# Kernel tuning notes

Measured on AMD Instinct MI355X. Metric: run time of the kernel, lower is better.

Reference implementation:

```python
import jax, jax.numpy as jnp
import numpy as np

N = 100000        # nodes
E = 1600000       # edges
D = 32            # hidden dim
C = 2             # num classes
NL = 4            # layer_num - 1 GIN layers
G = 512           # graphs in batch
BN_EPS = 1e-3     # keras BatchNormalization default epsilon


def setup_inputs() -> dict:
    key = jax.random.key(0)
    ks = jax.random.split(key, 16)
    s = 0.1
    return {
        "node_embeddings": jax.random.normal(ks[0], (N, D), dtype=jnp.float32),
        "edge_index": jax.random.randint(ks[1], (2, E), 0, N, dtype=jnp.int32),
        "batch": jnp.sort(jax.random.randint(ks[2], (N,), 0, G, dtype=jnp.int32)),
        # MLP inner dense + BN (per GIN layer)
        "W1": jax.random.normal(ks[3], (NL, D, D), dtype=jnp.float32) * s,
        "b1": jnp.zeros((NL, D), jnp.float32),
        "bn1_g": jnp.ones((NL, D), jnp.float32),
        "bn1_b": jnp.zeros((NL, D), jnp.float32),
        # MLP output dense
        "W2": jax.random.normal(ks[4], (NL, D, D), dtype=jnp.float32) * s,
        "b2": jnp.zeros((NL, D), jnp.float32),
        # ApplyNodeFunc BN
        "bn2_g": jnp.ones((NL, D), jnp.float32),
        "bn2_b": jnp.zeros((NL, D), jnp.float32),
        # outer per-layer BN
        "norm_g": jnp.ones((NL, D), jnp.float32),
        "norm_b": jnp.zeros((NL, D), jnp.float32),
        # readout heads: one Dense(num_classes) per hidden_rep level (layer_num of them)
        "dense_W": jax.random.normal(ks[5], (NL + 1, D, C), dtype=jnp.float32) * s,
        "dense_b": jnp.zeros((NL + 1, C), jnp.float32),
    }


def _bn(x, g, b):
    # inference-mode BatchNorm with init moving stats (mean=0, var=1)
    return x * (g / jnp.sqrt(1.0 + BN_EPS)) + b


def reference(node_embeddings, edge_index, batch, W1, b1, bn1_g, bn1_b,
              W2, b2, bn2_g, bn2_b, norm_g, norm_b, dense_W, dense_b):
    src, dst = edge_index[0], edge_index[1]
    h = node_embeddings
    hidden = [h]
    for i in range(NL):
        # GIN aggregation: (1+eps)*h + sum of neighbor features (eps=0)
        agg = jax.ops.segment_sum(h[src], dst, num_segments=N)  # [N, D]
        z = h + agg
        # ApplyNodeFunc: MLP (Dense->BN->ReLU->Dense) then BN + ReLU
        z = jax.nn.relu(_bn(z @ W1[i] + b1[i], bn1_g[i], bn1_b[i]))
        z = z @ W2[i] + b2[i]
        z = jax.nn.relu(_bn(z, bn2_g[i], bn2_b[i]))
        # outer norm + relu
        h = jax.nn.relu(_bn(z, norm_g[i], norm_b[i]))
        hidden.append(h)
    # readout: segment-sum pooling per hidden level, Dense(num_classes), summed
    score = jnp.zeros((G, C), dtype=node_embeddings.dtype)
    for i, hr in enumerate(hidden):
        pool = jax.ops.segment_sum(hr, batch, num_segments=G)  # [G, D]
        score = score + pool @ dense_W[i] + dense_b[i]
    return jax.nn.softmax(score, axis=-1)
```

## Files before the change

### kernel.cpp

```cpp
#include <hip/hip_runtime.h>

#define NN 100000
#define EE 1600000
#define DD 32
#define CC 2
#define NLAYERS 4
#define GG 512

#define BW 1024
#define NBUK ((NN + BW - 1) / BW)
#define CAP 24576
#define CH 8192
#define NPART ((EE + CH - 1) / CH)

__global__ void part_kernel(const int* __restrict__ ei,
                            int* __restrict__ gcur,
                            unsigned* __restrict__ part) {
    __shared__ unsigned sorted[CH];
    __shared__ unsigned char sbkt[CH];
    __shared__ int cnt[NBUK], offs[NBUK], cur[NBUK], gbs[NBUK];

    const int tid = threadIdx.x;
    const int eb  = blockIdx.x * CH;
    const int nch = min(CH, EE - eb);

    for (int b = tid; b < NBUK; b += 256) cnt[b] = 0;
    __syncthreads();
    for (int i = tid; i < nch; i += 256) {
        int dn = ei[EE + eb + i];
        atomicAdd(&cnt[dn >> 10], 1);
    }
    __syncthreads();
    if (tid == 0) {
        int o = 0;
        for (int b = 0; b < NBUK; ++b) { offs[b] = o; o += cnt[b]; }
    }
    __syncthreads();
    if (tid < NBUK) {
        cur[tid] = offs[tid];
        gbs[tid] = cnt[tid] ? atomicAdd(&gcur[tid], cnt[tid]) : 0;
    }
    __syncthreads();
    for (int i = tid; i < nch; i += 256) {
        int s  = ei[eb + i];
        int dn = ei[EE + eb + i];
        int b  = dn >> 10;
        unsigned pk = ((unsigned)(dn & (BW - 1)) << 17) | (unsigned)s;
        int p = atomicAdd(&cur[b], 1);
        sorted[p] = pk;
        sbkt[p]   = (unsigned char)b;
    }
    __syncthreads();
    for (int i = tid; i < nch; i += 256) {
        int b = sbkt[i];
        part[(size_t)b * CAP + gbs[b] + (i - offs[b])] = sorted[i];
    }
}

__global__ void bscan_kernel(const int* __restrict__ gcur,
                             int* __restrict__ bbase,
                             int* __restrict__ row_ptr) {
    if (threadIdx.x == 0 && blockIdx.x == 0) {
        int o = 0;
        for (int b = 0; b < NBUK; ++b) { bbase[b] = o; o += gcur[b]; }
        row_ptr[NN] = EE;
    }
}

__global__ void lcsr_kernel(const unsigned* __restrict__ part,
                            const int* __restrict__ gcur,
                            const int* __restrict__ bbase,
                            int* __restrict__ row_ptr,
                            int* __restrict__ csr_src) {
    __shared__ int hcnt[BW];
    __shared__ int a[2][BW];
    __shared__ int ccur[BW];
    const int t    = threadIdx.x;
    const int b    = blockIdx.x;
    const int cntb = gcur[b];
    const int base = bbase[b];
    const size_t pb = (size_t)b * CAP;

    hcnt[t] = 0;
    __syncthreads();
    for (int i = t; i < cntb; i += BW)
        atomicAdd(&hcnt[part[pb + i] >> 17], 1);
    __syncthreads();
    int x = hcnt[t];
    a[0][t] = x;
    __syncthreads();
    int cb = 0;
    for (int off = 1; off < BW; off <<= 1) {
        int v = a[cb][t];
        if (t >= off) v += a[cb][t - off];
        a[cb ^ 1][t] = v;
        cb ^= 1;
        __syncthreads();
    }
    const int excl = a[cb][t] - x;
    const int node = b * BW + t;
    if (node < NN) row_ptr[node] = base + excl;
    ccur[t] = excl;
    __syncthreads();
    for (int i = t; i < cntb; i += BW) {
        unsigned pk = part[pb + i];
        int dl  = pk >> 17;
        int pos = base + atomicAdd(&ccur[dl], 1);
        csr_src[pos] = (int)(pk & 0x1FFFFu);
    }
}

__global__ __launch_bounds__(256) void layer_kernel(
    const float* __restrict__ h_in, float* __restrict__ h_out,
    const int* __restrict__ row_ptr, const int* __restrict__ csr_src,
    const int* __restrict__ batch,
    const float* __restrict__ W1, const float* __restrict__ b1,
    const float* __restrict__ g1, const float* __restrict__ bt1,
    const float* __restrict__ W2, const float* __restrict__ b2,
    const float* __restrict__ g2, const float* __restrict__ bt2,
    const float* __restrict__ ng, const float* __restrict__ nb,
    const float* __restrict__ dWl, float* __restrict__ score) {
    __shared__ float sp[8 * DD];
    __shared__ float sdW[DD * CC];
    __shared__ float ss[GG * CC];
    __shared__ float zA[128][DD];
    __shared__ float z2loc[8][DD];

    const int tid = threadIdx.x;
    const int j = tid >> 5;
    const int d = tid & 31;

    float w1r[DD], w2r[DD];
    #pragma unroll
    for (int k = 0; k < DD; ++k) w1r[k] = W1[k * DD + d];
    #pragma unroll
    for (int k = 0; k < DD; ++k) w2r[k] = W2[k * DD + d];

    if (tid < DD) {
        sp[0 * DD + tid] = b1[tid];
        sp[1 * DD + tid] = g1[tid];
        sp[2 * DD + tid] = bt1[tid];
        sp[3 * DD + tid] = b2[tid];
        sp[4 * DD + tid] = g2[tid];
        sp[5 * DD + tid] = bt2[tid];
        sp[6 * DD + tid] = ng[tid];
        sp[7 * DD + tid] = nb[tid];
    }
    if (tid < DD * CC) sdW[tid] = dWl[tid];
    for (int i = tid; i < GG * CC; i += 256) ss[i] = 0.f;

    const float invs = 1.0f / sqrtf(1.001f);
    const int base = blockIdx.x * 128;

    for (int s = 0; s < 16; ++s) {
        const int n = base + j * 16 + s;
        if (n < NN) {
            float acc = h_in[(size_t)n * DD + d];
            int e = row_ptr[n];
            const int e1 = row_ptr[n + 1];
            for (; e + 4 <= e1; e += 4) {
                int s0 = csr_src[e + 0];
                int s1 = csr_src[e + 1];
                int s2 = csr_src[e + 2];
                int s3 = csr_src[e + 3];
                float v0 = h_in[(size_t)s0 * DD + d];
                float v1 = h_in[(size_t)s1 * DD + d];
                float v2 = h_in[(size_t)s2 * DD + d];
                float v3 = h_in[(size_t)s3 * DD + d];
                acc += v0 + v1 + v2 + v3;
            }
            for (; e < e1; ++e)
                acc += h_in[(size_t)csr_src[e] * DD + d];
            zA[j * 16 + s][d] = acc;
        }
    }
    __syncthreads();

    for (int s = 0; s < 16; ++s) {
        const int n = base + j * 16 + s;
        if (n >= NN) break;
        const int local = j * 16 + s;

        float a1 = sp[0 * DD + d];
        #pragma unroll
        for (int kk = 0; kk < DD; kk += 4) {
            const float4 zv = *reinterpret_cast<const float4*>(&zA[local][kk]);
            a1 += zv.x * w1r[kk] + zv.y * w1r[kk + 1] +
                  zv.z * w1r[kk + 2] + zv.w * w1r[kk + 3];
        }
        float v = fmaxf(a1 * (sp[1 * DD + d] * invs) + sp[2 * DD + d], 0.f);
        z2loc[j][d] = v;

        float a2 = sp[3 * DD + d];
        #pragma unroll
        for (int kk = 0; kk < DD; kk += 4) {
            const float4 zv = *reinterpret_cast<const float4*>(&z2loc[j][kk]);
            a2 += zv.x * w2r[kk] + zv.y * w2r[kk + 1] +
                  zv.z * w2r[kk + 2] + zv.w * w2r[kk + 3];
        }
        float w = fmaxf(a2 * (sp[4 * DD + d] * invs) + sp[5 * DD + d], 0.f);
        w = fmaxf(w * (sp[6 * DD + d] * invs) + sp[7 * DD + d], 0.f);
        h_out[(size_t)n * DD + d] = w;

        float p0 = w * sdW[d * CC + 0];
        float p1 = w * sdW[d * CC + 1];
        #pragma unroll
        for (int off = 16; off > 0; off >>= 1) {
            p0 += __shfl_xor(p0, off, 32);
            p1 += __shfl_xor(p1, off, 32);
        }
        if (d == 0) {
            int g = batch[n];
            atomicAdd(&ss[g * CC + 0], p0);
            atomicAdd(&ss[g * CC + 1], p1);
        }
    }
    __syncthreads();

    for (int i = tid; i < GG * CC; i += 256) {
        float v = ss[i];
        if (v != 0.f) atomicAdd(&score[i], v);
    }
}

__global__ void pool_kernel(const float* __restrict__ h,
                            const int* __restrict__ batch,
                            const float* __restrict__ Wd,
                            float* __restrict__ score) {
    __shared__ float ss[GG * CC];
    __shared__ float sW[DD * CC];
    const int tid = threadIdx.x;
    for (int i = tid; i < GG * CC; i += 256) ss[i] = 0.f;
    if (tid < DD * CC) sW[tid] = Wd[tid];
    __syncthreads();

    const int d = tid & 31;
    const int grp = tid >> 5;
    const int n0 = blockIdx.x * 512;
    const int n1 = (n0 + 512 < NN) ? (n0 + 512) : NN;

    for (int n = n0 + grp; n < n1; n += 8) {
        float v = h[(size_t)n * DD + d];
        float p0 = v * sW[d * CC + 0];
        float p1 = v * sW[d * CC + 1];
        #pragma unroll
        for (int off = 16; off > 0; off >>= 1) {
            p0 += __shfl_xor(p0, off, 32);
            p1 += __shfl_xor(p1, off, 32);
        }
        if (d == 0) {
            int g = batch[n];
            atomicAdd(&ss[g * CC + 0], p0);
            atomicAdd(&ss[g * CC + 1], p1);
        }
    }
    __syncthreads();

    for (int i = tid; i < GG * CC; i += 256) {
        float v = ss[i];
        if (v != 0.f) atomicAdd(&score[i], v);
    }
}

__global__ void softmax_kernel(const float* __restrict__ score,
                               const float* __restrict__ db,
                               float* __restrict__ out) {
    int g = blockIdx.x * blockDim.x + threadIdx.x;
    if (g >= GG) return;
    float bs0 = 0.f, bs1 = 0.f;
    #pragma unroll
    for (int i = 0; i <= NLAYERS; ++i) {
        bs0 += db[i * CC + 0];
        bs1 += db[i * CC + 1];
    }
    float s0 = score[g * CC + 0] + bs0;
    float s1 = score[g * CC + 1] + bs1;
    float m = fmaxf(s0, s1);
    float e0 = expf(s0 - m), e1 = expf(s1 - m);
    float inv = 1.f / (e0 + e1);
    out[g * CC + 0] = e0 * inv;
    out[g * CC + 1] = e1 * inv;
}

extern "C" void kernel_launch(void* const* d_in, const int* in_sizes, int n_in,
                              void* d_out, int out_size, void* d_ws, size_t ws_size,
                              hipStream_t stream) {
    (void)in_sizes; (void)n_in; (void)out_size; (void)ws_size;

    const float* node_emb = (const float*)d_in[0];
    const int*   ei       = (const int*)d_in[1];
    const int*   batch    = (const int*)d_in[2];
    const float* W1       = (const float*)d_in[3];
    const float* b1       = (const float*)d_in[4];
    const float* g1       = (const float*)d_in[5];
    const float* bt1      = (const float*)d_in[6];
    const float* W2       = (const float*)d_in[7];
    const float* b2       = (const float*)d_in[8];
    const float* g2       = (const float*)d_in[9];
    const float* bt2      = (const float*)d_in[10];
    const float* ng       = (const float*)d_in[11];
    const float* nb       = (const float*)d_in[12];
    const float* dW       = (const float*)d_in[13];
    const float* db       = (const float*)d_in[14];
    float* out = (float*)d_out;

    float* hA      = (float*)d_ws;
    float* hB      = hA + (size_t)NN * DD;
    unsigned* part = (unsigned*)hB;
    float* score   = hB + (size_t)NN * DD;
    int* row_ptr   = (int*)(score + GG * CC);
    int* csr_src   = row_ptr + NN + 2;
    int* gcur      = csr_src + EE;
    int* bbase     = gcur + 128;

    hipMemsetAsync(gcur, 0, 128 * sizeof(int), stream);
    hipMemsetAsync(score, 0, GG * CC * sizeof(float), stream);

    part_kernel<<<NPART, 256, 0, stream>>>(ei, gcur, part);
    bscan_kernel<<<1, 64, 0, stream>>>(gcur, bbase, row_ptr);
    lcsr_kernel<<<NBUK, BW, 0, stream>>>(part, gcur, bbase, row_ptr, csr_src);

    pool_kernel<<<(NN + 511) / 512, 256, 0, stream>>>(node_emb, batch, dW, score);

    const int layerGrid = (NN + 127) / 128;
    const float* cur_in = node_emb;
    float* bufs[2] = {hA, hB};
    for (int i = 0; i < NLAYERS; ++i) {
        float* o = bufs[i & 1];
        layer_kernel<<<layerGrid, 256, 0, stream>>>(
            cur_in, o, row_ptr, csr_src, batch,
            W1 + (size_t)i * DD * DD, b1 + i * DD, g1 + i * DD, bt1 + i * DD,
            W2 + (size_t)i * DD * DD, b2 + i * DD, g2 + i * DD, bt2 + i * DD,
            ng + i * DD, nb + i * DD,
            dW + (size_t)(i + 1) * DD * CC, score);
        cur_in = o;
    }

    softmax_kernel<<<(GG + 255) / 256, 256, 0, stream>>>(score, db, out);
}
```

Before: 467.4 us.

## Use finer CSR buckets, smaller partition chunks, and smaller layer tiles

Halves the destination bucket width to 512 nodes and cuts the partition chunk to 2048 edges, giving more partition blocks and smaller per-bucket local CSR builds. The layer kernel now handles 64 nodes per block instead of 128, doubling the grid, and unrolls the neighbor gather by 8 to keep more loads in flight. The aim is more parallelism and latency hiding in both the CSR build and the gather. In exchange, the per-block setup in the layer kernel (weight register loads, zeroing and flushing the shared score buffer) is repeated across twice as many blocks, and the bucket count in gcur now needs 196 slots, so its reservation grows to 256.

```diff
diff --git a/kernel.cpp b/kernel.cpp
--- a/kernel.cpp
+++ b/kernel.cpp
@@ -7,10 +7,11 @@
 #define NLAYERS 4
 #define GG 512
 
-#define BW 1024
+#define BSH 9
+#define BW 512
 #define NBUK ((NN + BW - 1) / BW)
-#define CAP 24576
-#define CH 8192
+#define CAP 12288
+#define CH 2048
 #define NPART ((EE + CH - 1) / CH)
 
 __global__ void part_kernel(const int* __restrict__ ei,
@@ -28,7 +29,7 @@
     __syncthreads();
     for (int i = tid; i < nch; i += 256) {
         int dn = ei[EE + eb + i];
-        atomicAdd(&cnt[dn >> 10], 1);
+        atomicAdd(&cnt[dn >> BSH], 1);
     }
     __syncthreads();
     if (tid == 0) {
@@ -44,7 +45,7 @@
     for (int i = tid; i < nch; i += 256) {
         int s  = ei[eb + i];
         int dn = ei[EE + eb + i];
-        int b  = dn >> 10;
+        int b  = dn >> BSH;
         unsigned pk = ((unsigned)(dn & (BW - 1)) << 17) | (unsigned)s;
         int p = atomicAdd(&cur[b], 1);
         sorted[p] = pk;
@@ -123,7 +124,7 @@
     __shared__ float sp[8 * DD];
     __shared__ float sdW[DD * CC];
     __shared__ float ss[GG * CC];
-    __shared__ float zA[128][DD];
+    __shared__ float zA[64][DD];
     __shared__ float z2loc[8][DD];
 
     const int tid = threadIdx.x;
@@ -150,36 +151,41 @@
     for (int i = tid; i < GG * CC; i += 256) ss[i] = 0.f;
 
     const float invs = 1.0f / sqrtf(1.001f);
-    const int base = blockIdx.x * 128;
-
-    for (int s = 0; s < 16; ++s) {
-        const int n = base + j * 16 + s;
+    const int base = blockIdx.x * 64;
+
+    for (int s = 0; s < 8; ++s) {
+        const int local = j * 8 + s;
+        const int n = base + local;
         if (n < NN) {
             float acc = h_in[(size_t)n * DD + d];
             int e = row_ptr[n];
             const int e1 = row_ptr[n + 1];
-            for (; e + 4 <= e1; e += 4) {
-                int s0 = csr_src[e + 0];
-                int s1 = csr_src[e + 1];
-                int s2 = csr_src[e + 2];
-                int s3 = csr_src[e + 3];
-                float v0 = h_in[(size_t)s0 * DD + d];
-                float v1 = h_in[(size_t)s1 * DD + d];
-                float v2 = h_in[(size_t)s2 * DD + d];
-                float v3 = h_in[(size_t)s3 * DD + d];
-                acc += v0 + v1 + v2 + v3;
+            for (; e + 8 <= e1; e += 8) {
+                int i0 = csr_src[e + 0], i1 = csr_src[e + 1];
+                int i2 = csr_src[e + 2], i3 = csr_src[e + 3];
+                int i4 = csr_src[e + 4], i5 = csr_src[e + 5];
+                int i6 = csr_src[e + 6], i7 = csr_src[e + 7];
+                float v0 = h_in[(size_t)i0 * DD + d];
+                float v1 = h_in[(size_t)i1 * DD + d];
+                float v2 = h_in[(size_t)i2 * DD + d];
+                float v3 = h_in[(size_t)i3 * DD + d];
+                float v4 = h_in[(size_t)i4 * DD + d];
+                float v5 = h_in[(size_t)i5 * DD + d];
+                float v6 = h_in[(size_t)i6 * DD + d];
+                float v7 = h_in[(size_t)i7 * DD + d];
+                acc += ((v0 + v1) + (v2 + v3)) + ((v4 + v5) + (v6 + v7));
             }
             for (; e < e1; ++e)
                 acc += h_in[(size_t)csr_src[e] * DD + d];
-            zA[j * 16 + s][d] = acc;
-        }
-    }
-    __syncthreads();
-
-    for (int s = 0; s < 16; ++s) {
-        const int n = base + j * 16 + s;
+            zA[local][d] = acc;
+        }
+    }
+    __syncthreads();
+
+    for (int s = 0; s < 8; ++s) {
+        const int local = j * 8 + s;
+        const int n = base + local;
         if (n >= NN) break;
-        const int local = j * 16 + s;
 
         float a1 = sp[0 * DD + d];
         #pragma unroll
@@ -311,9 +317,9 @@
     int* row_ptr   = (int*)(score + GG * CC);
     int* csr_src   = row_ptr + NN + 2;
     int* gcur      = csr_src + EE;
-    int* bbase     = gcur + 128;
-
-    hipMemsetAsync(gcur, 0, 128 * sizeof(int), stream);
+    int* bbase     = gcur + 256;
+
+    hipMemsetAsync(gcur, 0, 256 * sizeof(int), stream);
     hipMemsetAsync(score, 0, GG * CC * sizeof(float), stream);
 
     part_kernel<<<NPART, 256, 0, stream>>>(ei, gcur, part);
@@ -322,7 +328,7 @@
 
     pool_kernel<<<(NN + 511) / 512, 256, 0, stream>>>(node_emb, batch, dW, score);
 
-    const int layerGrid = (NN + 127) / 128;
+    const int layerGrid = (NN + 63) / 64;
     const float* cur_in = node_emb;
     float* bufs[2] = {hA, hB};
     for (int i = 0; i < NLAYERS; ++i) {
```

Result: no change. 472.2 us (+1.0%).
